# Optimization experiments

Measured on AMD Instinct MI355X. Metric: run time of the kernel, lower is better.

## Reference

```python
import jax, jax.numpy as jnp
import numpy as np

INTERVAL = 8
HEADS = 4
DIM = 64


def grid_shuffle(x, I):
    # rearrange 'b c (h i) (w j) -> (b i j) c h w' : stride-I residue grouping
    B, C, H, W = x.shape
    h, w = H // I, W // I
    x = x.reshape(B, C, h, I, w, I).transpose(0, 3, 5, 1, 2, 4)
    return x.reshape(B * I * I, C, h, w)


def grid_unshuffle(x, I, B):
    Bp, C, h, w = x.shape
    x = x.reshape(B, I, I, C, h, w).transpose(0, 3, 4, 1, 5, 2)
    return x.reshape(B, C, h * I, w * I)


def conv1x1(x, w, b):
    return jnp.einsum('oc,bchw->bohw', w, x) + b[None, :, None, None]


def pos_bias(h, w, W1, b1, W2, b2):
    # dynamic RPE: MLP over normalized relative coordinates -> [heads, N, N]
    ch = jnp.arange(h)
    cw = jnp.arange(w)
    coords = jnp.stack(jnp.meshgrid(ch, cw, indexing='ij'), -1).reshape(-1, 2).astype(jnp.float32)
    denom = jnp.array([max(h - 1, 1), max(w - 1, 1)], dtype=jnp.float32)
    rel = (coords[:, None, :] - coords[None, :, :]) / denom  # [N,N,2]
    hid = jax.nn.relu(rel @ W1 + b1)
    bias = hid @ W2 + b2  # [N,N,heads]
    return bias.transpose(2, 0, 1)


def mask_attn(q2d, k2d, v2d, bias, pw, pb, heads, scale):
    Bp, C, h, w = q2d.shape
    N, d = h * w, C // heads

    def to_tok(t):  # [Bp,C,h,w] -> [Bp,heads,N,d]
        return t.reshape(Bp, heads, d, N).transpose(0, 1, 3, 2)

    q, k, v = to_tok(q2d), to_tok(k2d), to_tok(v2d)
    attn = jnp.einsum('bhnd,bhmd->bhnm', q * scale, k) + bias[None]
    attn = jax.nn.softmax(attn, axis=-1)
    out = jnp.einsum('bhnm,bhmd->bhnd', attn, v)
    out2d = out.transpose(0, 1, 3, 2).reshape(Bp, C, h, w)
    return conv1x1(out2d, pw, pb)


def setup_inputs() -> dict:
    key = jax.random.key(0)
    ks = jax.random.split(key, 14)
    pos_hidden = DIM // 4  # 16
    s = 0.02
    return {
        'x': jax.random.normal(ks[0], (2, DIM, 160, 160), jnp.float32),
        'qkv_w': jax.random.normal(ks[1], (3 * DIM, DIM), jnp.float32) * s,
        'qkv_b': jnp.zeros((3 * DIM,), jnp.float32),
        'grid_w': jax.random.normal(ks[2], (DIM, DIM), jnp.float32) * s,
        'grid_b': jnp.zeros((DIM,), jnp.float32),
        'pos_w1': jax.random.normal(ks[3], (2, pos_hidden), jnp.float32) * s,
        'pos_b1': jnp.zeros((pos_hidden,), jnp.float32),
        'pos_w2': jax.random.normal(ks[4], (pos_hidden, HEADS), jnp.float32) * s,
        'pos_b2': jnp.zeros((HEADS,), jnp.float32),
        'proj1_w': jax.random.normal(ks[5], (DIM, DIM), jnp.float32) * s,
        'proj1_b': jnp.zeros((DIM,), jnp.float32),
        'proj2_w': jax.random.normal(ks[6], (DIM, DIM), jnp.float32) * s,
        'proj2_b': jnp.zeros((DIM,), jnp.float32),
    }


def reference(x, qkv_w, qkv_b, grid_w, grid_b, pos_w1, pos_b1, pos_w2, pos_b2,
              proj1_w, proj1_b, proj2_w, proj2_b):
    I = INTERVAL
    scale = (DIM // HEADS) ** -0.5
    B, C, H, W = x.shape
    qkv = conv1x1(x, qkv_w, qkv_b)
    x_grid = conv1x1(grid_shuffle(x, I), grid_w, grid_b)
    qkv = grid_shuffle(qkv, I)
    bias = pos_bias(H // I, W // I, pos_w1, pos_b1, pos_w2, pos_b2)
    q, k, v = jnp.split(qkv, 3, axis=1)
    out = mask_attn(x_grid, k, v, bias, proj1_w, proj1_b, HEADS, scale)
    out = mask_attn(q, x_grid, out, bias, proj2_w, proj2_b, HEADS, scale)
    return grid_unshuffle(out, I, B)
```

## Files before the change

### kernel.cpp

```cpp
#include <hip/hip_runtime.h>
#include <hip/hip_bf16.h>


#define N_TOK 400
#define NP    416
#define BP    128

typedef short bf16x8 __attribute__((ext_vector_type(8)));
typedef float f32x16 __attribute__((ext_vector_type(16)));

__device__ inline ushort f2bf(float f) {
    __hip_bfloat16 h = __float2bfloat16(f);
    return *reinterpret_cast<ushort*>(&h);
}
__device__ inline uint pk2(float a, float b) {
    return (uint)f2bf(a) | ((uint)f2bf(b) << 16);
}
__device__ inline bf16x8 ld16(const ushort* p) {
    union { uint4 q; bf16x8 v; } u;
    u.q = *reinterpret_cast<const uint4*>(p);
    return u.v;
}
__device__ inline float fast_exp2(float x) {
#if __has_builtin(__builtin_amdgcn_exp2f)
    return __builtin_amdgcn_exp2f(x);
#else
    return __expf(x * 0.6931471805599453f);
#endif
}

#define L2E 1.4426950408889634f

__global__ __launch_bounds__(256) void k_prepw(
    const float* __restrict__ qkv_w, const float* __restrict__ qkv_b,
    const float* __restrict__ grid_w, const float* __restrict__ grid_b,
    const float* __restrict__ p1w, const float* __restrict__ p2w,
    ushort* __restrict__ Wc, float* __restrict__ Bc,
    ushort* __restrict__ Wp1, ushort* __restrict__ Wp2)
{
    int t = blockIdx.x * 256 + threadIdx.x;
    if (t < 16384) {
        int oc = t >> 6, k = t & 63;
        float v = (oc < 192) ? qkv_w[oc * 64 + k] : grid_w[(oc - 192) * 64 + k];
        Wc[t] = f2bf(v);
    } else if (t < 16384 + 4096) {
        Wp1[t - 16384] = f2bf(p1w[t - 16384]);
    } else if (t < 16384 + 8192) {
        Wp2[t - 16384 - 4096] = f2bf(p2w[t - 16384 - 4096]);
    } else if (t < 16384 + 8192 + 256) {
        int oc = t - 16384 - 8192;
        Bc[oc] = (oc < 192) ? qkv_b[oc] : grid_b[oc - 192];
    }
}

__global__ __launch_bounds__(256) void k_biasF(
    const float* __restrict__ W1, const float* __restrict__ B1,
    const float* __restrict__ W2, const float* __restrict__ B2,
    float* __restrict__ biasF)
{
    int idx = blockIdx.x * 256 + threadIdx.x;
    if (idx >= 692224) return;
    int r = idx & 15, lane = (idx >> 4) & 63;
    int tile = idx >> 10;
    int mt = tile % 13, rem = tile / 13, qt = rem % 13, h = rem / 13;
    int n = qt * 32 + (lane & 31);
    int m = mt * 32 + (r & 3) + 8 * (r >> 2) + 4 * (lane >> 5);
    float val = 0.0f;
    if (n < 400 && m < 400) {
        float r0 = (float)(n / 20 - m / 20) * (1.0f / 19.0f);
        float r1 = (float)(n % 20 - m % 20) * (1.0f / 19.0f);
        float o = B2[h];
#pragma unroll
        for (int k = 0; k < 16; ++k) {
            float hh = r0 * W1[k] + r1 * W1[16 + k] + B1[k];
            hh = fmaxf(hh, 0.0f);
            o += hh * W2[k * 4 + h];
        }
        val = 4.0f * o;
    }
    biasF[idx] = val;
}

__global__ __launch_bounds__(256) void k_conv(
    const float* __restrict__ x, const ushort* __restrict__ Wc,
    const float* __restrict__ Bc,
    ushort* __restrict__ Qb, ushort* __restrict__ Kb,
    ushort* __restrict__ Vb, ushort* __restrict__ XGb)
{
    __shared__ __align__(16) ushort XL[32 * 64];
    int blk = blockIdx.x;
    int b = blk / 800, rem = blk % 800;
    int H0 = rem / 5, wt = rem % 5;
    int w0 = wt * 32;
    int tid = threadIdx.x;

    {
        int c = tid >> 2, q4 = tid & 3;
        const float* xr = x + ((size_t)(b * 64 + c) * 160 + H0) * 160 + w0 + q4 * 8;
        float4 f0 = *reinterpret_cast<const float4*>(xr);
        float4 f1 = *reinterpret_cast<const float4*>(xr + 4);
        char* base = reinterpret_cast<char*>(XL);
#pragma unroll
        for (int k = 0; k < 8; ++k) {
            float v = (k < 4) ? ((const float*)&f0)[k] : ((const float*)&f1)[k - 4];
            int p = q4 * 8 + k;
            int byt = p * 128 + ((2 * c) ^ ((p & 7) << 4));
            *reinterpret_cast<ushort*>(base + byt) = f2bf(v);
        }
    }

    int lane = tid & 63, w = tid >> 6;
    int l31 = lane & 31, hi = lane >> 5;

    bf16x8 wf[2][4];
#pragma unroll
    for (int nt = 0; nt < 2; ++nt)
#pragma unroll
        for (int kk = 0; kk < 4; ++kk)
            wf[nt][kk] = ld16(&Wc[(size_t)(w * 64 + nt * 32 + l31) * 64 + kk * 16 + hi * 8]);
    __syncthreads();

    f32x16 acc0 = 0.0f, acc1 = 0.0f;
    const char* base = reinterpret_cast<const char*>(XL);
#pragma unroll
    for (int kk = 0; kk < 4; ++kk) {
        int byt = l31 * 128 + (((kk * 32 + hi * 16)) ^ ((l31 & 7) << 4));
        bf16x8 xf;
        {
            union { uint4 q; bf16x8 v; } u;
            u.q = *reinterpret_cast<const uint4*>(base + byt);
            xf = u.v;
        }
        acc0 = __builtin_amdgcn_mfma_f32_32x32x16_bf16(wf[0][kk], xf, acc0, 0, 0, 0);
        acc1 = __builtin_amdgcn_mfma_f32_32x32x16_bf16(wf[1][kk], xf, acc1, 0, 0, 0);
    }

    int W0 = w0 + l31, ww = W0 >> 3, j = W0 & 7;
    int bp = b * 64 + (H0 & 7) * 8 + j;
    int n  = (H0 >> 3) * 20 + ww;
    ushort* outb = (w == 0) ? Qb : (w == 1) ? Kb : (w == 2) ? Vb : XGb;
    ushort* dst = outb + ((size_t)bp * NP + n) * 64;
#pragma unroll
    for (int nt = 0; nt < 2; ++nt) {
        const f32x16& a = nt ? acc1 : acc0;
#pragma unroll
        for (int g = 0; g < 4; ++g) {
            int cc = nt * 32 + 8 * g + 4 * hi;
            int oc = w * 64 + cc;
            uint2 uu;
            uu.x = pk2(a[4 * g + 0] + Bc[oc + 0], a[4 * g + 1] + Bc[oc + 1]);
            uu.y = pk2(a[4 * g + 2] + Bc[oc + 2], a[4 * g + 3] + Bc[oc + 3]);
            *reinterpret_cast<uint2*>(dst + cc) = uu;
        }
    }
}

__global__ __launch_bounds__(512, 4) void k_attn_mfma(
    const ushort* __restrict__ Qg, const ushort* __restrict__ Kg,
    const ushort* __restrict__ Vg, const float* __restrict__ biasF,
    ushort* __restrict__ O, float scale2)
{
    __shared__ ushort Ks[NP * 16];
    __shared__ ushort Vt[16 * 424];
    int blk = blockIdx.x;
    int bp = blk >> 2, h = blk & 3;
    int tid = threadIdx.x;

    const ushort* Ksrc = Kg + (size_t)bp * NP * 64 + h * 16;
    for (int i = tid; i < NP * 2; i += 512) {
        int row = i >> 1, half = i & 1;
        *reinterpret_cast<uint4*>(&Ks[row * 16 + half * 8]) =
            *reinterpret_cast<const uint4*>(&Ksrc[(size_t)row * 64 + half * 8]);
    }
    const ushort* Vsrc = Vg + (size_t)bp * NP * 64 + h * 16;
    {
        int c = tid & 15, r0 = tid >> 4;
        for (int row = r0; row < N_TOK; row += 32)
            Vt[c * 424 + row] = Vsrc[(size_t)row * 64 + c];
    }
    __syncthreads();

    int lane = tid & 63, w = tid >> 6;
    int l31 = lane & 31, hi = lane >> 5;

    for (int qt = w; qt < 13; qt += 8) {
        int qbase = qt * 32;
        bf16x8 qf = ld16(&Qg[((size_t)bp * NP + qbase + l31) * 64 + h * 16 + hi * 8]);
        f32x16 acc = 0.0f;
        float lrun = 0.0f;

        const float* bfr = biasF + ((size_t)(h * 169 + qt * 13)) * 1024 + lane * 16;
        float4 cb0 = *reinterpret_cast<const float4*>(bfr + 0);
        float4 cb1 = *reinterpret_cast<const float4*>(bfr + 4);
        float4 cb2 = *reinterpret_cast<const float4*>(bfr + 8);
        float4 cb3 = *reinterpret_cast<const float4*>(bfr + 12);

#pragma unroll
        for (int mt = 0; mt < 13; ++mt) {
            const int mbase = mt * 32;
            float4 nb0, nb1, nb2, nb3;
            if (mt < 12) {
                const float* nx = bfr + (size_t)(mt + 1) * 1024;
                nb0 = *reinterpret_cast<const float4*>(nx + 0);
                nb1 = *reinterpret_cast<const float4*>(nx + 4);
                nb2 = *reinterpret_cast<const float4*>(nx + 8);
                nb3 = *reinterpret_cast<const float4*>(nx + 12);
            }

            bf16x8 kf = ld16(&Ks[(mbase + l31) * 16 + hi * 8]);
            f32x16 cin;
            cin[0] = cb0.x; cin[1] = cb0.y; cin[2]  = cb0.z; cin[3]  = cb0.w;
            cin[4] = cb1.x; cin[5] = cb1.y; cin[6]  = cb1.z; cin[7]  = cb1.w;
            cin[8] = cb2.x; cin[9] = cb2.y; cin[10] = cb2.z; cin[11] = cb2.w;
            cin[12] = cb3.x; cin[13] = cb3.y; cin[14] = cb3.z; cin[15] = cb3.w;
            f32x16 sv = __builtin_amdgcn_mfma_f32_32x32x16_bf16(kf, qf, cin, 0, 0, 0);

            const int nv = (mt == 12) ? 8 : 16;
            float p[16];
#pragma unroll
            for (int r = 0; r < 16; ++r)
                if (r < nv) p[r] = fast_exp2(sv[r] * scale2);
            float rs;
            {
                float a = (p[0] + p[1]) + (p[2] + p[3]);
                float b = (p[4] + p[5]) + (p[6] + p[7]);
                rs = a + b;
                if (nv == 16) {
                    float c = (p[8] + p[9]) + (p[10] + p[11]);
                    float d = (p[12] + p[13]) + (p[14] + p[15]);
                    rs += c + d;
                }
            }
            lrun += rs;

            {
                uint c0 = pk2(p[0], p[1]), c1 = pk2(p[2], p[3]);
                uint c2 = pk2(p[4], p[5]), c3 = pk2(p[6], p[7]);
                asm("v_permlane32_swap_b32 %0, %1" : "+v"(c0), "+v"(c2));
                asm("v_permlane32_swap_b32 %0, %1" : "+v"(c1), "+v"(c3));
                union { uint u[4]; bf16x8 v; } A;
                A.u[0] = c0; A.u[1] = c1; A.u[2] = c2; A.u[3] = c3;
                bf16x8 vf = ld16(&Vt[(lane & 15) * 424 + mbase + hi * 8]);
                acc = __builtin_amdgcn_mfma_f32_32x32x16_bf16(A.v, vf, acc, 0, 0, 0);
            }
            if (mt < 12) {
                uint c4 = pk2(p[8], p[9]),  c5 = pk2(p[10], p[11]);
                uint c6 = pk2(p[12], p[13]), c7 = pk2(p[14], p[15]);
                asm("v_permlane32_swap_b32 %0, %1" : "+v"(c4), "+v"(c6));
                asm("v_permlane32_swap_b32 %0, %1" : "+v"(c5), "+v"(c7));
                union { uint u[4]; bf16x8 v; } A;
                A.u[0] = c4; A.u[1] = c5; A.u[2] = c6; A.u[3] = c7;
                bf16x8 vf = ld16(&Vt[(lane & 15) * 424 + mbase + 16 + hi * 8]);
                acc = __builtin_amdgcn_mfma_f32_32x32x16_bf16(A.v, vf, acc, 0, 0, 0);
            }
            cb0 = nb0; cb1 = nb1; cb2 = nb2; cb3 = nb3;
        }

        float tot = lrun + __shfl_xor(lrun, 32);
        float inv = 1.0f / tot;
        int dd = l31;
#pragma unroll
        for (int r = 0; r < 16; ++r) {
            int moff = (r & 3) + 8 * (r >> 2) + 4 * hi;
            int q = qbase + moff;
            float iv = __shfl(inv, moff);
            if (dd < 16 && q < N_TOK)
                O[((size_t)bp * N_TOK + q) * 64 + h * 16 + dd] = f2bf(acc[r] * iv);
        }
    }
}

template<int OUT_BF16>
__global__ __launch_bounds__(256) void k_proj(
    const ushort* __restrict__ In, const ushort* __restrict__ Wp,
    const float* __restrict__ Bv, void* __restrict__ Out)
{
    __shared__ __align__(16) ushort XL[128 * 64];
    size_t t0 = (size_t)blockIdx.x * 128;
    int tid = threadIdx.x;

    char* basec = reinterpret_cast<char*>(XL);
#pragma unroll
    for (int it = 0; it < 4; ++it) {
        int idx = tid + it * 256;
        int p = idx >> 3, c8 = idx & 7;
        uint4 v = *reinterpret_cast<const uint4*>(In + (t0 + p) * 64 + c8 * 8);
        int byt = p * 128 + ((c8 * 16) ^ ((p & 7) << 4));
        *reinterpret_cast<uint4*>(basec + byt) = v;
    }

    int lane = tid & 63, w = tid >> 6;
    int l31 = lane & 31, hi = lane >> 5;

    bf16x8 wf[2][4];
#pragma unroll
    for (int nt = 0; nt < 2; ++nt)
#pragma unroll
        for (int kk = 0; kk < 4; ++kk)
            wf[nt][kk] = ld16(&Wp[(size_t)(nt * 32 + l31) * 64 + kk * 16 + hi * 8]);
    __syncthreads();

    int prow = w * 32 + l31;
    f32x16 acc0 = 0.0f, acc1 = 0.0f;
#pragma unroll
    for (int kk = 0; kk < 4; ++kk) {
        int byt = prow * 128 + (((kk * 32 + hi * 16)) ^ ((prow & 7) << 4));
        union { uint4 q; bf16x8 v; } u;
        u.q = *reinterpret_cast<const uint4*>(basec + byt);
        acc0 = __builtin_amdgcn_mfma_f32_32x32x16_bf16(wf[0][kk], u.v, acc0, 0, 0, 0);
        acc1 = __builtin_amdgcn_mfma_f32_32x32x16_bf16(wf[1][kk], u.v, acc1, 0, 0, 0);
    }

    size_t t = t0 + prow;
    if (OUT_BF16) {
        int bp = (int)(t / 400), n = (int)(t % 400);
        ushort* dst = reinterpret_cast<ushort*>(Out) + ((size_t)bp * NP + n) * 64;
#pragma unroll
        for (int nt = 0; nt < 2; ++nt) {
            const f32x16& a = nt ? acc1 : acc0;
#pragma unroll
            for (int g = 0; g < 4; ++g) {
                int cc = nt * 32 + 8 * g + 4 * hi;
                uint2 uu;
                uu.x = pk2(a[4 * g + 0] + Bv[cc + 0], a[4 * g + 1] + Bv[cc + 1]);
                uu.y = pk2(a[4 * g + 2] + Bv[cc + 2], a[4 * g + 3] + Bv[cc + 3]);
                *reinterpret_cast<uint2*>(dst + cc) = uu;
            }
        }
    } else {
        float* dst = reinterpret_cast<float*>(Out) + t * 64;
#pragma unroll
        for (int nt = 0; nt < 2; ++nt) {
            const f32x16& a = nt ? acc1 : acc0;
#pragma unroll
            for (int g = 0; g < 4; ++g) {
                int cc = nt * 32 + 8 * g + 4 * hi;
                float4 f;
                f.x = a[4 * g + 0] + Bv[cc + 0];
                f.y = a[4 * g + 1] + Bv[cc + 1];
                f.z = a[4 * g + 2] + Bv[cc + 2];
                f.w = a[4 * g + 3] + Bv[cc + 3];
                *reinterpret_cast<float4*>(dst + cc) = f;
            }
        }
    }
}

__global__ __launch_bounds__(256) void k_unshuffle(
    const float* __restrict__ In, float* __restrict__ out)
{
    __shared__ __align__(16) float il[160 * 64];
    int blk = blockIdx.x;
    int b = blk / 160, rem = blk % 160, iI = rem / 20, hh = rem % 20;
    int tid = threadIdx.x;

    for (int idx = tid; idx < 2560; idx += 256) {
        int j = idx / 320, r2 = idx % 320, ww = r2 / 16, c4 = r2 % 16;
        int bp = b * 64 + iI * 8 + j;
        int n  = hh * 20 + ww;
        float4 v = reinterpret_cast<const float4*>(In + ((size_t)bp * 400 + n) * 64)[c4];
        reinterpret_cast<float4*>(&il[(ww * 8 + j) * 64])[c4] = v;
    }
    __syncthreads();

    int c = tid >> 2, q = tid & 3;
    int H0 = hh * 8 + iI;
    float* og = out + ((size_t)(b * 64 + c) * 160 + H0) * 160;
#pragma unroll
    for (int k = 0; k < 10; ++k) {
        int f = q + 4 * k;
        float4 v;
        v.x = il[(4 * f + 0) * 64 + c];
        v.y = il[(4 * f + 1) * 64 + c];
        v.z = il[(4 * f + 2) * 64 + c];
        v.w = il[(4 * f + 3) * 64 + c];
        reinterpret_cast<float4*>(og)[f] = v;
    }
}

extern "C" void kernel_launch(void* const* d_in, const int* in_sizes, int n_in,
                              void* d_out, int out_size, void* d_ws, size_t ws_size,
                              hipStream_t stream)
{
    const float* x      = (const float*)d_in[0];
    const float* qkv_w  = (const float*)d_in[1];
    const float* qkv_b  = (const float*)d_in[2];
    const float* grid_w = (const float*)d_in[3];
    const float* grid_b = (const float*)d_in[4];
    const float* pw1    = (const float*)d_in[5];
    const float* pb1    = (const float*)d_in[6];
    const float* pw2    = (const float*)d_in[7];
    const float* pb2    = (const float*)d_in[8];
    const float* p1w    = (const float*)d_in[9];
    const float* p1b    = (const float*)d_in[10];
    const float* p2w    = (const float*)d_in[11];
    const float* p2b    = (const float*)d_in[12];

    char* W = (char*)d_ws;
    float*  biasF = (float*)(W + 0);
    ushort* Wc    = (ushort*)(W + 2768896);
    ushort* Wp1   = (ushort*)(W + 2801664);
    ushort* Wp2   = (ushort*)(W + 2809856);
    float*  Bc    = (float*) (W + 2818048);
    const size_t BASE2 = 2819072;
    const size_t BB = (size_t)BP * NP * 64 * 2;
    ushort* Qb = (ushort*)(W + BASE2);
    ushort* Kb = (ushort*)(W + BASE2 + 1 * BB);
    ushort* Vb = (ushort*)(W + BASE2 + 2 * BB);
    ushort* XG = (ushort*)(W + BASE2 + 3 * BB);
    ushort* P1 = (ushort*)(W + BASE2 + 4 * BB);
    const size_t OB = (size_t)BP * N_TOK * 64 * 2;
    ushort* O1 = (ushort*)(W + BASE2 + 5 * BB);
    ushort* O2 = (ushort*)(W + BASE2 + 5 * BB + OB);
    float*  OF = (float*)(W + BASE2);
    float*  out = (float*)d_out;

    const float scale2 = 0.25f * L2E;

    k_prepw<<<97, 256, 0, stream>>>(qkv_w, qkv_b, grid_w, grid_b, p1w, p2w, Wc, Bc, Wp1, Wp2);
    k_biasF<<<2704, 256, 0, stream>>>(pw1, pb1, pw2, pb2, biasF);
    k_conv<<<1600, 256, 0, stream>>>(x, Wc, Bc, Qb, Kb, Vb, XG);
    k_attn_mfma<<<512, 512, 0, stream>>>(XG, Kb, Vb, biasF, O1, scale2);
    k_proj<1><<<400, 256, 0, stream>>>(O1, Wp1, p1b, (void*)P1);
    k_attn_mfma<<<512, 512, 0, stream>>>(Qb, XG, P1, biasF, O2, scale2);
    k_proj<0><<<400, 256, 0, stream>>>(O2, Wp2, p2b, (void*)OF);
    k_unshuffle<<<320, 256, 0, stream>>>(OF, out);
}
```

Before: 128.1 us.

## Split attention blocks per query half, fuse prep kernels, bf16 final projection output

Each attention work item (batch, head) now runs as two 256-thread blocks, each handling half the query tiles. Every wave processes two query tiles at once and shares the K/V fragment loads between them, and the V transpose is loaded with vectorized 16-byte reads. The weight-prep and position-bias kernels are merged into one launch. The final projection now writes bf16 instead of fp32, and unshuffle reads bf16, which halves that intermediate traffic. The price is a second round of K/V staging per head, since both blocks load it, plus a precision loss on the last intermediate.

```diff
diff --git a/kernel.cpp b/kernel.cpp
--- a/kernel.cpp
+++ b/kernel.cpp
@@ -12,6 +12,9 @@
 __device__ inline ushort f2bf(float f) {
     __hip_bfloat16 h = __float2bfloat16(f);
     return *reinterpret_cast<ushort*>(&h);
+}
+__device__ inline float bf2f(ushort u) {
+    union { uint i; float f; } v; v.i = (uint)u << 16; return v.f;
 }
 __device__ inline uint pk2(float a, float b) {
     return (uint)f2bf(a) | ((uint)f2bf(b) << 16);
@@ -31,54 +34,53 @@
 
 #define L2E 1.4426950408889634f
 
-__global__ __launch_bounds__(256) void k_prepw(
+__global__ __launch_bounds__(256) void k_prep(
+    const float* __restrict__ W1, const float* __restrict__ B1,
+    const float* __restrict__ W2, const float* __restrict__ B2,
     const float* __restrict__ qkv_w, const float* __restrict__ qkv_b,
     const float* __restrict__ grid_w, const float* __restrict__ grid_b,
     const float* __restrict__ p1w, const float* __restrict__ p2w,
-    ushort* __restrict__ Wc, float* __restrict__ Bc,
+    float* __restrict__ biasF, ushort* __restrict__ Wc, float* __restrict__ Bc,
     ushort* __restrict__ Wp1, ushort* __restrict__ Wp2)
 {
-    int t = blockIdx.x * 256 + threadIdx.x;
-    if (t < 16384) {
-        int oc = t >> 6, k = t & 63;
-        float v = (oc < 192) ? qkv_w[oc * 64 + k] : grid_w[(oc - 192) * 64 + k];
-        Wc[t] = f2bf(v);
-    } else if (t < 16384 + 4096) {
-        Wp1[t - 16384] = f2bf(p1w[t - 16384]);
-    } else if (t < 16384 + 8192) {
-        Wp2[t - 16384 - 4096] = f2bf(p2w[t - 16384 - 4096]);
-    } else if (t < 16384 + 8192 + 256) {
-        int oc = t - 16384 - 8192;
-        Bc[oc] = (oc < 192) ? qkv_b[oc] : grid_b[oc - 192];
-    }
-}
-
-__global__ __launch_bounds__(256) void k_biasF(
-    const float* __restrict__ W1, const float* __restrict__ B1,
-    const float* __restrict__ W2, const float* __restrict__ B2,
-    float* __restrict__ biasF)
-{
-    int idx = blockIdx.x * 256 + threadIdx.x;
-    if (idx >= 692224) return;
-    int r = idx & 15, lane = (idx >> 4) & 63;
-    int tile = idx >> 10;
-    int mt = tile % 13, rem = tile / 13, qt = rem % 13, h = rem / 13;
-    int n = qt * 32 + (lane & 31);
-    int m = mt * 32 + (r & 3) + 8 * (r >> 2) + 4 * (lane >> 5);
-    float val = 0.0f;
-    if (n < 400 && m < 400) {
-        float r0 = (float)(n / 20 - m / 20) * (1.0f / 19.0f);
-        float r1 = (float)(n % 20 - m % 20) * (1.0f / 19.0f);
-        float o = B2[h];
-#pragma unroll
-        for (int k = 0; k < 16; ++k) {
-            float hh = r0 * W1[k] + r1 * W1[16 + k] + B1[k];
-            hh = fmaxf(hh, 0.0f);
-            o += hh * W2[k * 4 + h];
-        }
-        val = 4.0f * o;
-    }
-    biasF[idx] = val;
+    int blk = blockIdx.x;
+    if (blk < 2704) {
+        int idx = blk * 256 + threadIdx.x;
+        if (idx >= 692224) return;
+        int r = idx & 15, lane = (idx >> 4) & 63;
+        int tile = idx >> 10;
+        int mt = tile % 13, rem = tile / 13, qt = rem % 13, h = rem / 13;
+        int n = qt * 32 + (lane & 31);
+        int m = mt * 32 + (r & 3) + 8 * (r >> 2) + 4 * (lane >> 5);
+        float val = 0.0f;
+        if (n < 400 && m < 400) {
+            float r0 = (float)(n / 20 - m / 20) * (1.0f / 19.0f);
+            float r1 = (float)(n % 20 - m % 20) * (1.0f / 19.0f);
+            float o = B2[h];
+#pragma unroll
+            for (int k = 0; k < 16; ++k) {
+                float hh = r0 * W1[k] + r1 * W1[16 + k] + B1[k];
+                hh = fmaxf(hh, 0.0f);
+                o += hh * W2[k * 4 + h];
+            }
+            val = 4.0f * o;
+        }
+        biasF[idx] = val;
+    } else {
+        int t = (blk - 2704) * 256 + threadIdx.x;
+        if (t < 16384) {
+            int oc = t >> 6, k = t & 63;
+            float v = (oc < 192) ? qkv_w[oc * 64 + k] : grid_w[(oc - 192) * 64 + k];
+            Wc[t] = f2bf(v);
+        } else if (t < 16384 + 4096) {
+            Wp1[t - 16384] = f2bf(p1w[t - 16384]);
+        } else if (t < 16384 + 8192) {
+            Wp2[t - 16384 - 4096] = f2bf(p2w[t - 16384 - 4096]);
+        } else if (t < 16384 + 8192 + 256) {
+            int oc = t - 16384 - 8192;
+            Bc[oc] = (oc < 192) ? qkv_b[oc] : grid_b[oc - 192];
+        }
+    }
 }
 
 __global__ __launch_bounds__(256) void k_conv(
@@ -155,7 +157,7 @@
     }
 }
 
-__global__ __launch_bounds__(512, 4) void k_attn_mfma(
+__global__ __launch_bounds__(256, 4) void k_attn_mfma(
     const ushort* __restrict__ Qg, const ushort* __restrict__ Kg,
     const ushort* __restrict__ Vg, const float* __restrict__ biasF,
     ushort* __restrict__ O, float scale2)
@@ -163,85 +165,95 @@
     __shared__ ushort Ks[NP * 16];
     __shared__ ushort Vt[16 * 424];
     int blk = blockIdx.x;
-    int bp = blk >> 2, h = blk & 3;
+    int bp = blk >> 3, h = (blk >> 1) & 3, sub = blk & 1;
+    int qt0 = sub ? 7 : 0;
+    int cnt = sub ? 6 : 7;
     int tid = threadIdx.x;
 
     const ushort* Ksrc = Kg + (size_t)bp * NP * 64 + h * 16;
-    for (int i = tid; i < NP * 2; i += 512) {
-        int row = i >> 1, half = i & 1;
-        *reinterpret_cast<uint4*>(&Ks[row * 16 + half * 8]) =
-            *reinterpret_cast<const uint4*>(&Ksrc[(size_t)row * 64 + half * 8]);
+#pragma unroll
+    for (int it = 0; it < 4; ++it) {
+        int i = tid + it * 256;
+        if (i < NP * 2) {
+            int row = i >> 1, half = i & 1;
+            *reinterpret_cast<uint4*>(&Ks[row * 16 + half * 8]) =
+                *reinterpret_cast<const uint4*>(&Ksrc[(size_t)row * 64 + half * 8]);
+        }
     }
     const ushort* Vsrc = Vg + (size_t)bp * NP * 64 + h * 16;
-    {
-        int c = tid & 15, r0 = tid >> 4;
-        for (int row = r0; row < N_TOK; row += 32)
-            Vt[c * 424 + row] = Vsrc[(size_t)row * 64 + c];
+#pragma unroll
+    for (int it = 0; it < 4; ++it) {
+        int i = tid + it * 256;
+        if (i < 800) {
+            int row = i >> 1, hf = i & 1;
+            uint4 v = *reinterpret_cast<const uint4*>(&Vsrc[(size_t)row * 64 + hf * 8]);
+            const ushort* pv = reinterpret_cast<const ushort*>(&v);
+#pragma unroll
+            for (int k = 0; k < 8; ++k)
+                Vt[(hf * 8 + k) * 424 + row] = pv[k];
+        }
     }
     __syncthreads();
 
     int lane = tid & 63, w = tid >> 6;
     int l31 = lane & 31, hi = lane >> 5;
 
-    for (int qt = w; qt < 13; qt += 8) {
-        int qbase = qt * 32;
-        bf16x8 qf = ld16(&Qg[((size_t)bp * NP + qbase + l31) * 64 + h * 16 + hi * 8]);
-        f32x16 acc = 0.0f;
-        float lrun = 0.0f;
-
-        const float* bfr = biasF + ((size_t)(h * 169 + qt * 13)) * 1024 + lane * 16;
-        float4 cb0 = *reinterpret_cast<const float4*>(bfr + 0);
-        float4 cb1 = *reinterpret_cast<const float4*>(bfr + 4);
-        float4 cb2 = *reinterpret_cast<const float4*>(bfr + 8);
-        float4 cb3 = *reinterpret_cast<const float4*>(bfr + 12);
-
-#pragma unroll
-        for (int mt = 0; mt < 13; ++mt) {
-            const int mbase = mt * 32;
-            float4 nb0, nb1, nb2, nb3;
-            if (mt < 12) {
-                const float* nx = bfr + (size_t)(mt + 1) * 1024;
-                nb0 = *reinterpret_cast<const float4*>(nx + 0);
-                nb1 = *reinterpret_cast<const float4*>(nx + 4);
-                nb2 = *reinterpret_cast<const float4*>(nx + 8);
-                nb3 = *reinterpret_cast<const float4*>(nx + 12);
-            }
-
-            bf16x8 kf = ld16(&Ks[(mbase + l31) * 16 + hi * 8]);
+    int qtA = qt0 + w;
+    bool have2 = (w + 4) < cnt;
+    int qtB = have2 ? (qt0 + w + 4) : qtA;
+    int qbA = qtA * 32, qbB = qtB * 32;
+
+    bf16x8 qfA = ld16(&Qg[((size_t)bp * NP + qbA + l31) * 64 + h * 16 + hi * 8]);
+    bf16x8 qfB = ld16(&Qg[((size_t)bp * NP + qbB + l31) * 64 + h * 16 + hi * 8]);
+    f32x16 accA = 0.0f, accB = 0.0f;
+    float lA = 0.0f, lB = 0.0f;
+    const float* bfrA = biasF + ((size_t)(h * 169 + qtA * 13)) * 1024 + lane * 16;
+    const float* bfrB = biasF + ((size_t)(h * 169 + qtB * 13)) * 1024 + lane * 16;
+
+#pragma unroll
+    for (int mt = 0; mt < 13; ++mt) {
+        const int mbase = mt * 32;
+        bf16x8 kf = ld16(&Ks[(mbase + l31) * 16 + hi * 8]);
+        bf16x8 vf0 = ld16(&Vt[(lane & 15) * 424 + mbase + hi * 8]);
+        bf16x8 vf1;
+        if (mt < 12) vf1 = ld16(&Vt[(lane & 15) * 424 + mbase + 16 + hi * 8]);
+        const int nv = (mt == 12) ? 8 : 16;
+
+        {
+            const float* bx = bfrA + (size_t)mt * 1024;
+            float4 c0 = *reinterpret_cast<const float4*>(bx + 0);
+            float4 c1 = *reinterpret_cast<const float4*>(bx + 4);
+            float4 c2 = *reinterpret_cast<const float4*>(bx + 8);
+            float4 c3 = *reinterpret_cast<const float4*>(bx + 12);
             f32x16 cin;
-            cin[0] = cb0.x; cin[1] = cb0.y; cin[2]  = cb0.z; cin[3]  = cb0.w;
-            cin[4] = cb1.x; cin[5] = cb1.y; cin[6]  = cb1.z; cin[7]  = cb1.w;
-            cin[8] = cb2.x; cin[9] = cb2.y; cin[10] = cb2.z; cin[11] = cb2.w;
-            cin[12] = cb3.x; cin[13] = cb3.y; cin[14] = cb3.z; cin[15] = cb3.w;
-            f32x16 sv = __builtin_amdgcn_mfma_f32_32x32x16_bf16(kf, qf, cin, 0, 0, 0);
-
-            const int nv = (mt == 12) ? 8 : 16;
+            cin[0] = c0.x; cin[1] = c0.y; cin[2]  = c0.z; cin[3]  = c0.w;
+            cin[4] = c1.x; cin[5] = c1.y; cin[6]  = c1.z; cin[7]  = c1.w;
+            cin[8] = c2.x; cin[9] = c2.y; cin[10] = c2.z; cin[11] = c2.w;
+            cin[12] = c3.x; cin[13] = c3.y; cin[14] = c3.z; cin[15] = c3.w;
+            f32x16 sv = __builtin_amdgcn_mfma_f32_32x32x16_bf16(kf, qfA, cin, 0, 0, 0);
             float p[16];
 #pragma unroll
             for (int r = 0; r < 16; ++r)
                 if (r < nv) p[r] = fast_exp2(sv[r] * scale2);
-            float rs;
             {
                 float a = (p[0] + p[1]) + (p[2] + p[3]);
                 float b = (p[4] + p[5]) + (p[6] + p[7]);
-                rs = a + b;
+                float rs = a + b;
                 if (nv == 16) {
                     float c = (p[8] + p[9]) + (p[10] + p[11]);
                     float d = (p[12] + p[13]) + (p[14] + p[15]);
                     rs += c + d;
                 }
-            }
-            lrun += rs;
-
+                lA += rs;
+            }
             {
-                uint c0 = pk2(p[0], p[1]), c1 = pk2(p[2], p[3]);
-                uint c2 = pk2(p[4], p[5]), c3 = pk2(p[6], p[7]);
-                asm("v_permlane32_swap_b32 %0, %1" : "+v"(c0), "+v"(c2));
-                asm("v_permlane32_swap_b32 %0, %1" : "+v"(c1), "+v"(c3));
+                uint c4 = pk2(p[0], p[1]), c5 = pk2(p[2], p[3]);
+                uint c6 = pk2(p[4], p[5]), c7 = pk2(p[6], p[7]);
+                asm("v_permlane32_swap_b32 %0, %1" : "+v"(c4), "+v"(c6));
+                asm("v_permlane32_swap_b32 %0, %1" : "+v"(c5), "+v"(c7));
                 union { uint u[4]; bf16x8 v; } A;
-                A.u[0] = c0; A.u[1] = c1; A.u[2] = c2; A.u[3] = c3;
-                bf16x8 vf = ld16(&Vt[(lane & 15) * 424 + mbase + hi * 8]);
-                acc = __builtin_amdgcn_mfma_f32_32x32x16_bf16(A.v, vf, acc, 0, 0, 0);
+                A.u[0] = c4; A.u[1] = c5; A.u[2] = c6; A.u[3] = c7;
+                accA = __builtin_amdgcn_mfma_f32_32x32x16_bf16(A.v, vf0, accA, 0, 0, 0);
             }
             if (mt < 12) {
                 uint c4 = pk2(p[8], p[9]),  c5 = pk2(p[10], p[11]);
@@ -250,30 +262,88 @@
                 asm("v_permlane32_swap_b32 %0, %1" : "+v"(c5), "+v"(c7));
                 union { uint u[4]; bf16x8 v; } A;
                 A.u[0] = c4; A.u[1] = c5; A.u[2] = c6; A.u[3] = c7;
-                bf16x8 vf = ld16(&Vt[(lane & 15) * 424 + mbase + 16 + hi * 8]);
-                acc = __builtin_amdgcn_mfma_f32_32x32x16_bf16(A.v, vf, acc, 0, 0, 0);
-            }
-            cb0 = nb0; cb1 = nb1; cb2 = nb2; cb3 = nb3;
-        }
-
-        float tot = lrun + __shfl_xor(lrun, 32);
+                accA = __builtin_amdgcn_mfma_f32_32x32x16_bf16(A.v, vf1, accA, 0, 0, 0);
+            }
+        }
+
+        if (have2) {
+            const float* bx = bfrB + (size_t)mt * 1024;
+            float4 c0 = *reinterpret_cast<const float4*>(bx + 0);
+            float4 c1 = *reinterpret_cast<const float4*>(bx + 4);
+            float4 c2 = *reinterpret_cast<const float4*>(bx + 8);
+            float4 c3 = *reinterpret_cast<const float4*>(bx + 12);
+            f32x16 cin;
+            cin[0] = c0.x; cin[1] = c0.y; cin[2]  = c0.z; cin[3]  = c0.w;
+            cin[4] = c1.x; cin[5] = c1.y; cin[6]  = c1.z; cin[7]  = c1.w;
+            cin[8] = c2.x; cin[9] = c2.y; cin[10] = c2.z; cin[11] = c2.w;
+            cin[12] = c3.x; cin[13] = c3.y; cin[14] = c3.z; cin[15] = c3.w;
+            f32x16 sv = __builtin_amdgcn_mfma_f32_32x32x16_bf16(kf, qfB, cin, 0, 0, 0);
+            float p[16];
+#pragma unroll
+            for (int r = 0; r < 16; ++r)
+                if (r < nv) p[r] = fast_exp2(sv[r] * scale2);
+            {
+                float a = (p[0] + p[1]) + (p[2] + p[3]);
+                float b = (p[4] + p[5]) + (p[6] + p[7]);
+                float rs = a + b;
+                if (nv == 16) {
+                    float c = (p[8] + p[9]) + (p[10] + p[11]);
+                    float d = (p[12] + p[13]) + (p[14] + p[15]);
+                    rs += c + d;
+                }
+                lB += rs;
+            }
+            {
+                uint c4 = pk2(p[0], p[1]), c5 = pk2(p[2], p[3]);
+                uint c6 = pk2(p[4], p[5]), c7 = pk2(p[6], p[7]);
+                asm("v_permlane32_swap_b32 %0, %1" : "+v"(c4), "+v"(c6));
+                asm("v_permlane32_swap_b32 %0, %1" : "+v"(c5), "+v"(c7));
+                union { uint u[4]; bf16x8 v; } A;
+                A.u[0] = c4; A.u[1] = c5; A.u[2] = c6; A.u[3] = c7;
+                accB = __builtin_amdgcn_mfma_f32_32x32x16_bf16(A.v, vf0, accB, 0, 0, 0);
+            }
+            if (mt < 12) {
+                uint c4 = pk2(p[8], p[9]),  c5 = pk2(p[10], p[11]);
+                uint c6 = pk2(p[12], p[13]), c7 = pk2(p[14], p[15]);
+                asm("v_permlane32_swap_b32 %0, %1" : "+v"(c4), "+v"(c6));
+                asm("v_permlane32_swap_b32 %0, %1" : "+v"(c5), "+v"(c7));
+                union { uint u[4]; bf16x8 v; } A;
+                A.u[0] = c4; A.u[1] = c5; A.u[2] = c6; A.u[3] = c7;
+                accB = __builtin_amdgcn_mfma_f32_32x32x16_bf16(A.v, vf1, accB, 0, 0, 0);
+            }
+        }
+    }
+
+    {
+        float tot = lA + __shfl_xor(lA, 32);
         float inv = 1.0f / tot;
-        int dd = l31;
 #pragma unroll
         for (int r = 0; r < 16; ++r) {
             int moff = (r & 3) + 8 * (r >> 2) + 4 * hi;
-            int q = qbase + moff;
+            int q = qbA + moff;
             float iv = __shfl(inv, moff);
-            if (dd < 16 && q < N_TOK)
-                O[((size_t)bp * N_TOK + q) * 64 + h * 16 + dd] = f2bf(acc[r] * iv);
-        }
-    }
-}
-
-template<int OUT_BF16>
+            if (l31 < 16 && q < N_TOK)
+                O[((size_t)bp * 400 + q) * 64 + h * 16 + l31] = f2bf(accA[r] * iv);
+        }
+    }
+    if (have2) {
+        float tot = lB + __shfl_xor(lB, 32);
+        float inv = 1.0f / tot;
+#pragma unroll
+        for (int r = 0; r < 16; ++r) {
+            int moff = (r & 3) + 8 * (r >> 2) + 4 * hi;
+            int q = qbB + moff;
+            float iv = __shfl(inv, moff);
+            if (l31 < 16 && q < N_TOK)
+                O[((size_t)bp * 400 + q) * 64 + h * 16 + l31] = f2bf(accB[r] * iv);
+        }
+    }
+}
+
+template<int MODE>
 __global__ __launch_bounds__(256) void k_proj(
     const ushort* __restrict__ In, const ushort* __restrict__ Wp,
-    const float* __restrict__ Bv, void* __restrict__ Out)
+    const float* __restrict__ Bv, ushort* __restrict__ Out)
 {
     __shared__ __align__(16) ushort XL[128 * 64];
     size_t t0 = (size_t)blockIdx.x * 128;
@@ -312,54 +382,41 @@
     }
 
     size_t t = t0 + prow;
-    if (OUT_BF16) {
+    ushort* dst;
+    if (MODE == 0) {
         int bp = (int)(t / 400), n = (int)(t % 400);
-        ushort* dst = reinterpret_cast<ushort*>(Out) + ((size_t)bp * NP + n) * 64;
-#pragma unroll
-        for (int nt = 0; nt < 2; ++nt) {
-            const f32x16& a = nt ? acc1 : acc0;
-#pragma unroll
-            for (int g = 0; g < 4; ++g) {
-                int cc = nt * 32 + 8 * g + 4 * hi;
-                uint2 uu;
-                uu.x = pk2(a[4 * g + 0] + Bv[cc + 0], a[4 * g + 1] + Bv[cc + 1]);
-                uu.y = pk2(a[4 * g + 2] + Bv[cc + 2], a[4 * g + 3] + Bv[cc + 3]);
-                *reinterpret_cast<uint2*>(dst + cc) = uu;
-            }
-        }
+        dst = Out + ((size_t)bp * NP + n) * 64;
     } else {
-        float* dst = reinterpret_cast<float*>(Out) + t * 64;
-#pragma unroll
-        for (int nt = 0; nt < 2; ++nt) {
-            const f32x16& a = nt ? acc1 : acc0;
-#pragma unroll
-            for (int g = 0; g < 4; ++g) {
-                int cc = nt * 32 + 8 * g + 4 * hi;
-                float4 f;
-                f.x = a[4 * g + 0] + Bv[cc + 0];
-                f.y = a[4 * g + 1] + Bv[cc + 1];
-                f.z = a[4 * g + 2] + Bv[cc + 2];
-                f.w = a[4 * g + 3] + Bv[cc + 3];
-                *reinterpret_cast<float4*>(dst + cc) = f;
-            }
+        dst = Out + t * 64;
+    }
+#pragma unroll
+    for (int nt = 0; nt < 2; ++nt) {
+        const f32x16& a = nt ? acc1 : acc0;
+#pragma unroll
+        for (int g = 0; g < 4; ++g) {
+            int cc = nt * 32 + 8 * g + 4 * hi;
+            uint2 uu;
+            uu.x = pk2(a[4 * g + 0] + Bv[cc + 0], a[4 * g + 1] + Bv[cc + 1]);
+            uu.y = pk2(a[4 * g + 2] + Bv[cc + 2], a[4 * g + 3] + Bv[cc + 3]);
+            *reinterpret_cast<uint2*>(dst + cc) = uu;
         }
     }
 }
 
 __global__ __launch_bounds__(256) void k_unshuffle(
-    const float* __restrict__ In, float* __restrict__ out)
-{
-    __shared__ __align__(16) float il[160 * 64];
+    const ushort* __restrict__ In, float* __restrict__ out)
+{
+    __shared__ __align__(16) ushort il[160 * 64];
     int blk = blockIdx.x;
     int b = blk / 160, rem = blk % 160, iI = rem / 20, hh = rem % 20;
     int tid = threadIdx.x;
 
-    for (int idx = tid; idx < 2560; idx += 256) {
-        int j = idx / 320, r2 = idx % 320, ww = r2 / 16, c4 = r2 % 16;
+    for (int idx = tid; idx < 1280; idx += 256) {
+        int j = idx / 160, r2 = idx % 160, ww = r2 / 8, c8 = r2 % 8;
         int bp = b * 64 + iI * 8 + j;
         int n  = hh * 20 + ww;
-        float4 v = reinterpret_cast<const float4*>(In + ((size_t)bp * 400 + n) * 64)[c4];
-        reinterpret_cast<float4*>(&il[(ww * 8 + j) * 64])[c4] = v;
+        uint4 v = reinterpret_cast<const uint4*>(In + ((size_t)bp * 400 + n) * 64)[c8];
+        reinterpret_cast<uint4*>(&il[(ww * 8 + j) * 64])[c8] = v;
     }
     __syncthreads();
 
@@ -370,10 +427,10 @@
     for (int k = 0; k < 10; ++k) {
         int f = q + 4 * k;
         float4 v;
-        v.x = il[(4 * f + 0) * 64 + c];
-        v.y = il[(4 * f + 1) * 64 + c];
-        v.z = il[(4 * f + 2) * 64 + c];
-        v.w = il[(4 * f + 3) * 64 + c];
+        v.x = bf2f(il[(4 * f + 0) * 64 + c]);
+        v.y = bf2f(il[(4 * f + 1) * 64 + c]);
+        v.z = bf2f(il[(4 * f + 2) * 64 + c]);
+        v.w = bf2f(il[(4 * f + 3) * 64 + c]);
         reinterpret_cast<float4*>(og)[f] = v;
     }
 }
@@ -409,20 +466,20 @@
     ushort* Vb = (ushort*)(W + BASE2 + 2 * BB);
     ushort* XG = (ushort*)(W + BASE2 + 3 * BB);
     ushort* P1 = (ushort*)(W + BASE2 + 4 * BB);
-    const size_t OB = (size_t)BP * N_TOK * 64 * 2;
+    const size_t OB = (size_t)BP * 400 * 64 * 2;
     ushort* O1 = (ushort*)(W + BASE2 + 5 * BB);
     ushort* O2 = (ushort*)(W + BASE2 + 5 * BB + OB);
-    float*  OF = (float*)(W + BASE2);
+    ushort* OFb = O1;
     float*  out = (float*)d_out;
 
     const float scale2 = 0.25f * L2E;
 
-    k_prepw<<<97, 256, 0, stream>>>(qkv_w, qkv_b, grid_w, grid_b, p1w, p2w, Wc, Bc, Wp1, Wp2);
-    k_biasF<<<2704, 256, 0, stream>>>(pw1, pb1, pw2, pb2, biasF);
+    k_prep<<<2801, 256, 0, stream>>>(pw1, pb1, pw2, pb2, qkv_w, qkv_b, grid_w, grid_b,
+                                     p1w, p2w, biasF, Wc, Bc, Wp1, Wp2);
     k_conv<<<1600, 256, 0, stream>>>(x, Wc, Bc, Qb, Kb, Vb, XG);
-    k_attn_mfma<<<512, 512, 0, stream>>>(XG, Kb, Vb, biasF, O1, scale2);
-    k_proj<1><<<400, 256, 0, stream>>>(O1, Wp1, p1b, (void*)P1);
-    k_attn_mfma<<<512, 512, 0, stream>>>(Qb, XG, P1, biasF, O2, scale2);
-    k_proj<0><<<400, 256, 0, stream>>>(O2, Wp2, p2b, (void*)OF);
-    k_unshuffle<<<320, 256, 0, stream>>>(OF, out);
-}
+    k_attn_mfma<<<1024, 256, 0, stream>>>(XG, Kb, Vb, biasF, O1, scale2);
+    k_proj<0><<<400, 256, 0, stream>>>(O1, Wp1, p1b, P1);
+    k_attn_mfma<<<1024, 256, 0, stream>>>(Qb, XG, P1, biasF, O2, scale2);
+    k_proj<1><<<400, 256, 0, stream>>>(O2, Wp2, p2b, OFb);
+    k_unshuffle<<<320, 256, 0, stream>>>(OFb, out);
+}
```

After: 209.5 us. 1.63x slower.
